# Optimization experiments

Hardware: AMD Instinct MI355X
Metric: run time of the kernel (lower is better)

## Reference

```python
import jax, jax.numpy as jnp
import numpy as np

KS = 11  # conv kernel size, padding = KS//2 -> SAME


def setup_inputs() -> dict:
    key = jax.random.key(0)
    ks = jax.random.split(key, 6)
    B, H, W = 16, 256, 256
    x = jax.random.uniform(ks[0], (B, 1, H, W), jnp.float32)
    # conv_same(1,1,ks=11,bias=False) -> OIHW kernel [1,1,11,11]
    K = jax.random.normal(ks[1], (1, 1, KS, KS), jnp.float32) * (1.0 / KS)
    # rule: Linear(1,10) -> ReLU -> Linear(10,10) -> ReLU -> Linear(10,1), all with bias
    w1 = jax.random.normal(ks[2], (10, 1), jnp.float32) * 0.5
    b1 = jnp.zeros((10,), jnp.float32)
    w2 = jax.random.normal(ks[3], (10, 10), jnp.float32) * 0.3
    b2 = jnp.zeros((10,), jnp.float32)
    w3 = jax.random.normal(ks[4], (1, 10), jnp.float32) * 0.3
    b3 = jnp.zeros((1,), jnp.float32)
    return {"x": x, "K": K, "w1": w1, "b1": b1, "w2": w2, "b2": b2,
            "w3": w3, "b3": b3, "steps": 16}


def reference(x, K, w1, b1, w2, b2, w3, b3, steps):
    # One NCA step: 11x11 single-channel conv -> pointwise 3-layer MLP on the
    # channel dim (Permute makes Linear act per-pixel) -> clipped residual add.
    def step(xc, _):
        out = jax.lax.conv_general_dilated(
            xc, K, window_strides=(1, 1), padding="SAME",
            dimension_numbers=("NCHW", "OIHW", "NCHW"))  # [B,1,H,W]
        v = out[:, 0]                                   # [B,H,W]
        h = jax.nn.relu(v[..., None] * w1[:, 0] + b1)   # [B,H,W,10]
        h = jax.nn.relu(jnp.einsum("bhwi,oi->bhwo", h, w2) + b2)
        y = jnp.einsum("bhwi,oi->bhwo", h, w3) + b3     # [B,H,W,1]
        xn = jnp.clip(xc + jnp.moveaxis(y, -1, 1), 0.0, 1.0)
        return xn, xn

    _, seq = jax.lax.scan(step, x, None, length=steps)
    # torch returns a list [x0, x1, ..., x_steps]; we stack it.
    return jnp.concatenate([x[None], seq], axis=0)  # [steps+1, B, 1, H, W]
```

## Files before the change

kernel.cpp:

```cpp
#include <hip/hip_runtime.h>


#define HH 256
#define WW 256
#define BB 16
#define TH 16
#define TW 64
#define SH (TH + 10)
#define SW (TW + 10)
#define SWP 76
#define SLAB (BB * HH * WW)

__global__ __launch_bounds__(256) void nca_copy_x(const float* __restrict__ x,
                                                  float* __restrict__ out) {
    int i = (blockIdx.x * 256 + threadIdx.x) * 4;
    *(float4*)(out + i) = *(const float4*)(x + i);
}

__global__ __launch_bounds__(256) void nca_step(
    const float* __restrict__ src, float* __restrict__ dst,
    const float* __restrict__ Kk,
    const float* __restrict__ w1, const float* __restrict__ b1,
    const float* __restrict__ w2, const float* __restrict__ b2,
    const float* __restrict__ w3, const float* __restrict__ b3) {
    __shared__ __align__(16) float s[SH * SWP];

    const int tid = threadIdx.x;
    const int b   = blockIdx.z;
    const int gy0 = blockIdx.y * TH;
    const int gx0 = blockIdx.x * TW;
    const float* img = src + b * HH * WW;

    for (int i = tid; i < SH * SW; i += 256) {
        int r = i / SW, c = i - r * SW;
        int gy = gy0 - 5 + r, gx = gx0 - 5 + c;
        float v = 0.f;
        if (gy >= 0 && gy < HH && gx >= 0 && gx < WW) v = img[gy * WW + gx];
        s[r * SWP + c] = v;
    }
    __syncthreads();

    const int tx = tid & 15, ty = tid >> 4;
    const int x0 = tx * 4;

    float acc0 = 0.f, acc1 = 0.f, acc2 = 0.f, acc3 = 0.f;
#pragma unroll
    for (int ky = 0; ky < 11; ++ky) {
        const float* row = &s[(ty + ky) * SWP + x0];
        float win[16];
        *(float4*)(win + 0)  = *(const float4*)(row + 0);
        *(float4*)(win + 4)  = *(const float4*)(row + 4);
        *(float4*)(win + 8)  = *(const float4*)(row + 8);
        *(float2*)(win + 12) = *(const float2*)(row + 12);
#pragma unroll
        for (int kx = 0; kx < 11; ++kx) {
            float kv = Kk[ky * 11 + kx];
            acc0 = fmaf(win[kx + 0], kv, acc0);
            acc1 = fmaf(win[kx + 1], kv, acc1);
            acc2 = fmaf(win[kx + 2], kv, acc2);
            acc3 = fmaf(win[kx + 3], kv, acc3);
        }
    }

    const float b3v = b3[0];
    float vacc[4] = {acc0, acc1, acc2, acc3};
    float res[4];
#pragma unroll
    for (int p = 0; p < 4; ++p) {
        float v = vacc[p];
        float h1[10];
#pragma unroll
        for (int i = 0; i < 10; ++i)
            h1[i] = fmaxf(fmaf(v, w1[i], b1[i]), 0.f);
        float y = b3v;
#pragma unroll
        for (int o = 0; o < 10; ++o) {
            float a = b2[o];
#pragma unroll
            for (int i = 0; i < 10; ++i)
                a = fmaf(h1[i], w2[o * 10 + i], a);
            y = fmaf(fmaxf(a, 0.f), w3[o], y);
        }
        float xc = s[(ty + 5) * SWP + x0 + 5 + p];
        res[p] = fminf(fmaxf(xc + y, 0.f), 1.f);
    }

    float* orow = dst + b * HH * WW + (gy0 + ty) * WW + gx0 + x0;
    *(float4*)orow = make_float4(res[0], res[1], res[2], res[3]);
}

extern "C" void kernel_launch(void* const* d_in, const int* in_sizes, int n_in,
                              void* d_out, int out_size, void* d_ws, size_t ws_size,
                              hipStream_t stream) {
    const float* x  = (const float*)d_in[0];
    const float* Kk = (const float*)d_in[1];
    const float* w1 = (const float*)d_in[2];
    const float* b1 = (const float*)d_in[3];
    const float* w2 = (const float*)d_in[4];
    const float* b2 = (const float*)d_in[5];
    const float* w3 = (const float*)d_in[6];
    const float* b3 = (const float*)d_in[7];
    float* out = (float*)d_out;

    nca_copy_x<<<SLAB / (256 * 4), 256, 0, stream>>>(x, out);

    dim3 grid(WW / TW, HH / TH, BB);
    for (int k = 0; k < 16; ++k) {
        nca_step<<<grid, 256, 0, stream>>>(out + (size_t)k * SLAB,
                                           out + (size_t)(k + 1) * SLAB,
                                           Kk, w1, b1, w2, b2, w3, b3);
    }
}
```

Before: 289.2 us.

## Enlarge tile to 32x64 with 8 outputs per thread and float4 halo loads

```diff
diff --git a/kernel.cpp b/kernel.cpp
--- a/kernel.cpp
+++ b/kernel.cpp
@@ -4,11 +4,10 @@
 #define HH 256
 #define WW 256
 #define BB 16
-#define TH 16
+#define TH 32
 #define TW 64
 #define SH (TH + 10)
-#define SW (TW + 10)
-#define SWP 76
+#define SW 80
 #define SLAB (BB * HH * WW)
 
 __global__ __launch_bounds__(256) void nca_copy_x(const float* __restrict__ x,
@@ -23,7 +22,7 @@
     const float* __restrict__ w1, const float* __restrict__ b1,
     const float* __restrict__ w2, const float* __restrict__ b2,
     const float* __restrict__ w3, const float* __restrict__ b3) {
-    __shared__ __align__(16) float s[SH * SWP];
+    __shared__ __align__(16) float s[SH * SW];
 
     const int tid = threadIdx.x;
     const int b   = blockIdx.z;
@@ -31,62 +30,85 @@
     const int gx0 = blockIdx.x * TW;
     const float* img = src + b * HH * WW;
 
-    for (int i = tid; i < SH * SW; i += 256) {
-        int r = i / SW, c = i - r * SW;
-        int gy = gy0 - 5 + r, gx = gx0 - 5 + c;
-        float v = 0.f;
-        if (gy >= 0 && gy < HH && gx >= 0 && gx < WW) v = img[gy * WW + gx];
-        s[r * SWP + c] = v;
+    for (int t = tid; t < SH * (SW / 4); t += 256) {
+        int r = t / (SW / 4), c = t - r * (SW / 4);
+        int gy = gy0 - 5 + r;
+        int gx = gx0 - 8 + c * 4;
+        float4 v = make_float4(0.f, 0.f, 0.f, 0.f);
+        if ((unsigned)gy < HH && (unsigned)gx < WW)
+            v = *(const float4*)(img + gy * WW + gx);
+        *(float4*)(s + r * SW + c * 4) = v;
     }
     __syncthreads();
 
-    const int tx = tid & 15, ty = tid >> 4;
-    const int x0 = tx * 4;
+    const int tx = tid & 7, ty = tid >> 3;
+    const int x0 = tx * 8;
 
-    float acc0 = 0.f, acc1 = 0.f, acc2 = 0.f, acc3 = 0.f;
+    float acc[8] = {0, 0, 0, 0, 0, 0, 0, 0};
+    float xc[8];
 #pragma unroll
     for (int ky = 0; ky < 11; ++ky) {
-        const float* row = &s[(ty + ky) * SWP + x0];
-        float win[16];
+        const float* row = &s[(ty + ky) * SW + x0];
+        float win[24];
         *(float4*)(win + 0)  = *(const float4*)(row + 0);
         *(float4*)(win + 4)  = *(const float4*)(row + 4);
         *(float4*)(win + 8)  = *(const float4*)(row + 8);
-        *(float2*)(win + 12) = *(const float2*)(row + 12);
+        *(float4*)(win + 12) = *(const float4*)(row + 12);
+        *(float4*)(win + 16) = *(const float4*)(row + 16);
+        *(float4*)(win + 20) = *(const float4*)(row + 20);
+        if (ky == 5) {
+#pragma unroll
+            for (int p = 0; p < 8; ++p) xc[p] = win[p + 8];
+        }
+        const float* krow = Kk + ky * 11;
+        float kr[11];
+#pragma unroll
+        for (int j = 0; j < 11; ++j) kr[j] = krow[j];
 #pragma unroll
         for (int kx = 0; kx < 11; ++kx) {
-            float kv = Kk[ky * 11 + kx];
-            acc0 = fmaf(win[kx + 0], kv, acc0);
-            acc1 = fmaf(win[kx + 1], kv, acc1);
-            acc2 = fmaf(win[kx + 2], kv, acc2);
-            acc3 = fmaf(win[kx + 3], kv, acc3);
+#pragma unroll
+            for (int p = 0; p < 8; ++p)
+                acc[p] = fmaf(win[kx + p + 3], kr[kx], acc[p]);
         }
     }
 
     const float b3v = b3[0];
-    float vacc[4] = {acc0, acc1, acc2, acc3};
-    float res[4];
+    float res[8];
 #pragma unroll
-    for (int p = 0; p < 4; ++p) {
-        float v = vacc[p];
-        float h1[10];
+    for (int g = 0; g < 2; ++g) {
+        float h1[4][10];
 #pragma unroll
-        for (int i = 0; i < 10; ++i)
-            h1[i] = fmaxf(fmaf(v, w1[i], b1[i]), 0.f);
-        float y = b3v;
+        for (int i = 0; i < 10; ++i) {
+            float w1i = w1[i], b1i = b1[i];
+#pragma unroll
+            for (int p = 0; p < 4; ++p)
+                h1[p][i] = fmaxf(fmaf(acc[g * 4 + p], w1i, b1i), 0.f);
+        }
+        float yv[4] = {b3v, b3v, b3v, b3v};
 #pragma unroll
         for (int o = 0; o < 10; ++o) {
-            float a = b2[o];
+            float b2o = b2[o];
+            float a[4] = {b2o, b2o, b2o, b2o};
 #pragma unroll
-            for (int i = 0; i < 10; ++i)
-                a = fmaf(h1[i], w2[o * 10 + i], a);
-            y = fmaf(fmaxf(a, 0.f), w3[o], y);
+            for (int i = 0; i < 10; ++i) {
+                float w = w2[o * 10 + i];
+#pragma unroll
+                for (int p = 0; p < 4; ++p)
+                    a[p] = fmaf(h1[p][i], w, a[p]);
+            }
+            float w3o = w3[o];
+#pragma unroll
+            for (int p = 0; p < 4; ++p)
+                yv[p] = fmaf(fmaxf(a[p], 0.f), w3o, yv[p]);
         }
-        float xc = s[(ty + 5) * SWP + x0 + 5 + p];
-        res[p] = fminf(fmaxf(xc + y, 0.f), 1.f);
+#pragma unroll
+        for (int p = 0; p < 4; ++p)
+            res[g * 4 + p] = fminf(fmaxf(xc[g * 4 + p] + yv[p], 0.f), 1.f);
     }
 
     float* orow = dst + b * HH * WW + (gy0 + ty) * WW + gx0 + x0;
-    *(float4*)orow = make_float4(res[0], res[1], res[2], res[3]);
+    *(float4*)(orow + 0) = *(float4*)(res + 0);
+    *(float4*)(orow + 4) = *(float4*)(res + 4);
 }
 
 extern "C" void kernel_launch(void* const* d_in, const int* in_sizes, int n_in,
```

Measured after the change: 382.1 us. +32.1%, slower.

## Collapse zero-bias ReLU MLP to piecewise-linear and retile conv with swizzled smem

Applied to the files above, without the earlier changes.

```diff
diff --git a/kernel.cpp b/kernel.cpp
--- a/kernel.cpp
+++ b/kernel.cpp
@@ -4,12 +4,13 @@
 #define HH 256
 #define WW 256
 #define BB 16
-#define TH 16
 #define TW 64
-#define SH (TH + 10)
-#define SW (TW + 10)
-#define SWP 76
+#define TH 32
+#define SROWS 42
+#define NBLKX 21
+#define SSTR 96
 #define SLAB (BB * HH * WW)
+#define NSTEPS 16
 
 __global__ __launch_bounds__(256) void nca_copy_x(const float* __restrict__ x,
                                                   float* __restrict__ out) {
@@ -17,13 +18,43 @@
     *(float4*)(out + i) = *(const float4*)(x + i);
 }
 
+__device__ float mlp_full(float v, const float* w1, const float* b1,
+                          const float* w2, const float* b2,
+                          const float* w3, const float* b3) {
+    float h1[10];
+#pragma unroll
+    for (int i = 0; i < 10; ++i) h1[i] = fmaxf(fmaf(v, w1[i], b1[i]), 0.f);
+    float y = b3[0];
+#pragma unroll
+    for (int o = 0; o < 10; ++o) {
+        float a = b2[o];
+#pragma unroll
+        for (int i = 0; i < 10; ++i) a = fmaf(h1[i], w2[o * 10 + i], a);
+        y = fmaf(fmaxf(a, 0.f), w3[o], y);
+    }
+    return y;
+}
+
+__global__ void nca_coef(const float* __restrict__ w1, const float* __restrict__ b1,
+                         const float* __restrict__ w2, const float* __restrict__ b2,
+                         const float* __restrict__ w3, const float* __restrict__ b3,
+                         float* __restrict__ cf) {
+    if (threadIdx.x == 0) {
+        bool zero = (b3[0] == 0.f);
+        for (int i = 0; i < 10; ++i) zero = zero && (b1[i] == 0.f) && (b2[i] == 0.f);
+        cf[0] = mlp_full(1.f, w1, b1, w2, b2, w3, b3);
+        cf[1] = mlp_full(-1.f, w1, b1, w2, b2, w3, b3);
+        cf[2] = zero ? 1.f : 0.f;
+    }
+}
+
 __global__ __launch_bounds__(256) void nca_step(
     const float* __restrict__ src, float* __restrict__ dst,
-    const float* __restrict__ Kk,
+    const float* __restrict__ cf, const float* __restrict__ Kk,
     const float* __restrict__ w1, const float* __restrict__ b1,
     const float* __restrict__ w2, const float* __restrict__ b2,
     const float* __restrict__ w3, const float* __restrict__ b3) {
-    __shared__ __align__(16) float s[SH * SWP];
+    __shared__ __align__(16) float s[SROWS * SSTR];
 
     const int tid = threadIdx.x;
     const int b   = blockIdx.z;
@@ -31,62 +62,111 @@
     const int gx0 = blockIdx.x * TW;
     const float* img = src + b * HH * WW;
 
-    for (int i = tid; i < SH * SW; i += 256) {
-        int r = i / SW, c = i - r * SW;
-        int gy = gy0 - 5 + r, gx = gx0 - 5 + c;
-        float v = 0.f;
-        if (gy >= 0 && gy < HH && gx >= 0 && gx < WW) v = img[gy * WW + gx];
-        s[r * SWP + c] = v;
+    for (int t = tid; t < SROWS * NBLKX; t += 256) {
+        int r = t / NBLKX, c = t - r * NBLKX;
+        int gy = gy0 - 5 + r, gx = gx0 - 8 + c * 4;
+        float4 v = make_float4(0.f, 0.f, 0.f, 0.f);
+        if ((unsigned)gy < HH && (unsigned)gx < WW)
+            v = *(const float4*)(img + gy * WW + gx);
+        int pb = c ^ ((r >> 1) & 3);
+        *(float4*)(s + r * SSTR + pb * 4) = v;
     }
     __syncthreads();
 
     const int tx = tid & 15, ty = tid >> 4;
+    const int rb = ty * 2;
     const int x0 = tx * 4;
 
-    float acc0 = 0.f, acc1 = 0.f, acc2 = 0.f, acc3 = 0.f;
+    float acc[2][4];
 #pragma unroll
-    for (int ky = 0; ky < 11; ++ky) {
-        const float* row = &s[(ty + ky) * SWP + x0];
-        float win[16];
-        *(float4*)(win + 0)  = *(const float4*)(row + 0);
-        *(float4*)(win + 4)  = *(const float4*)(row + 4);
-        *(float4*)(win + 8)  = *(const float4*)(row + 8);
-        *(float2*)(win + 12) = *(const float2*)(row + 12);
+    for (int r = 0; r < 2; ++r)
 #pragma unroll
-        for (int kx = 0; kx < 11; ++kx) {
-            float kv = Kk[ky * 11 + kx];
-            acc0 = fmaf(win[kx + 0], kv, acc0);
-            acc1 = fmaf(win[kx + 1], kv, acc1);
-            acc2 = fmaf(win[kx + 2], kv, acc2);
-            acc3 = fmaf(win[kx + 3], kv, acc3);
+        for (int p = 0; p < 4; ++p) acc[r][p] = 0.f;
+
+    {
+        float ka[55];
+#pragma unroll
+        for (int j = 0; j < 55; ++j) ka[j] = Kk[j];
+#pragma unroll
+        for (int W = 0; W < 6; ++W) {
+            int SR = rb + W;
+            int sw = (SR >> 1) & 3;
+            const float* rowp = s + SR * SSTR;
+            float win[20];
+#pragma unroll
+            for (int i = 0; i < 5; ++i)
+                *(float4*)(win + 4 * i) = *(const float4*)(rowp + ((tx + i) ^ sw) * 4);
+#pragma unroll
+            for (int r = 0; r < 2; ++r) {
+                const int ky = W - r;
+                if (ky >= 0 && ky <= 4) {
+#pragma unroll
+                    for (int kx = 0; kx < 11; ++kx) {
+                        float kv = ka[ky * 11 + kx];
+#pragma unroll
+                        for (int p = 0; p < 4; ++p)
+                            acc[r][p] = fmaf(win[p + 3 + kx], kv, acc[r][p]);
+                    }
+                }
+            }
+        }
+    }
+    {
+        float kb[66];
+#pragma unroll
+        for (int j = 0; j < 66; ++j) kb[j] = Kk[55 + j];
+#pragma unroll
+        for (int W = 5; W < 12; ++W) {
+            int SR = rb + W;
+            int sw = (SR >> 1) & 3;
+            const float* rowp = s + SR * SSTR;
+            float win[20];
+#pragma unroll
+            for (int i = 0; i < 5; ++i)
+                *(float4*)(win + 4 * i) = *(const float4*)(rowp + ((tx + i) ^ sw) * 4);
+#pragma unroll
+            for (int r = 0; r < 2; ++r) {
+                const int ky = W - r;
+                if (ky >= 5 && ky <= 10) {
+#pragma unroll
+                    for (int kx = 0; kx < 11; ++kx) {
+                        float kv = kb[(ky - 5) * 11 + kx];
+#pragma unroll
+                        for (int p = 0; p < 4; ++p)
+                            acc[r][p] = fmaf(win[p + 3 + kx], kv, acc[r][p]);
+                    }
+                }
+            }
         }
     }
 
-    const float b3v = b3[0];
-    float vacc[4] = {acc0, acc1, acc2, acc3};
-    float res[4];
+    const float A = cf[0], B = cf[1];
+    const bool fast = cf[2] > 0.5f;
+    float* dimg = dst + b * HH * WW;
 #pragma unroll
-    for (int p = 0; p < 4; ++p) {
-        float v = vacc[p];
-        float h1[10];
+    for (int r = 0; r < 2; ++r) {
+        int SRc = rb + r + 5;
+        int sw = (SRc >> 1) & 3;
+        const float4 xcv = *(const float4*)(s + SRc * SSTR + ((tx + 2) ^ sw) * 4);
+        const float xc[4] = {xcv.x, xcv.y, xcv.z, xcv.w};
+        float res[4];
+        if (fast) {
 #pragma unroll
-        for (int i = 0; i < 10; ++i)
-            h1[i] = fmaxf(fmaf(v, w1[i], b1[i]), 0.f);
-        float y = b3v;
+            for (int p = 0; p < 4; ++p) {
+                float v = acc[r][p];
+                float y = (v >= 0.f) ? v * A : (-v) * B;
+                res[p] = fminf(fmaxf(xc[p] + y, 0.f), 1.f);
+            }
+        } else {
 #pragma unroll
-        for (int o = 0; o < 10; ++o) {
-            float a = b2[o];
-#pragma unroll
-            for (int i = 0; i < 10; ++i)
-                a = fmaf(h1[i], w2[o * 10 + i], a);
-            y = fmaf(fmaxf(a, 0.f), w3[o], y);
+            for (int p = 0; p < 4; ++p) {
+                float y = mlp_full(acc[r][p], w1, b1, w2, b2, w3, b3);
+                res[p] = fminf(fmaxf(xc[p] + y, 0.f), 1.f);
+            }
         }
-        float xc = s[(ty + 5) * SWP + x0 + 5 + p];
-        res[p] = fminf(fmaxf(xc + y, 0.f), 1.f);
+        *(float4*)(dimg + (gy0 + rb + r) * WW + gx0 + x0) =
+            make_float4(res[0], res[1], res[2], res[3]);
     }
-
-    float* orow = dst + b * HH * WW + (gy0 + ty) * WW + gx0 + x0;
-    *(float4*)orow = make_float4(res[0], res[1], res[2], res[3]);
 }
 
 extern "C" void kernel_launch(void* const* d_in, const int* in_sizes, int n_in,
@@ -101,13 +181,15 @@
     const float* w3 = (const float*)d_in[6];
     const float* b3 = (const float*)d_in[7];
     float* out = (float*)d_out;
+    float* cf  = (float*)d_ws;
 
+    nca_coef<<<1, 64, 0, stream>>>(w1, b1, w2, b2, w3, b3, cf);
     nca_copy_x<<<SLAB / (256 * 4), 256, 0, stream>>>(x, out);
 
     dim3 grid(WW / TW, HH / TH, BB);
-    for (int k = 0; k < 16; ++k) {
+    for (int k = 0; k < NSTEPS; ++k) {
         nca_step<<<grid, 256, 0, stream>>>(out + (size_t)k * SLAB,
                                            out + (size_t)(k + 1) * SLAB,
-                                           Kk, w1, b1, w2, b2, w3, b3);
+                                           cf, Kk, w1, b1, w2, b2, w3, b3);
     }
 }
```

Result: slower. 389.8 us (+34.8%).
